# Performance work log

Measured on AMD Instinct MI355X. Metric: run time of the kernel, lower is better.

Reference implementation:

```python
import jax, jax.numpy as jnp
import numpy as np
from jax import lax

B, L, F = 32, 2048, 76   # batch, seq_len, feat_dim
H = 128                  # conv hidden channels
D = 128                  # prototype dim (last 1x1 conv)
P = 128                  # number of prototypes
CLASS_SIZE = 2


def setup_inputs() -> dict:
    key = jax.random.key(0)
    ks = jax.random.split(key, 8)
    w = lambda k, shape: jax.random.normal(k, shape, jnp.float32) * 0.05
    return {
        "x": jax.random.normal(ks[0], (B, L, F), jnp.float32),
        "W1": w(ks[1], (H, F, 5)), "b1": jnp.zeros((H,), jnp.float32),
        "W2": w(ks[2], (H, H, 5)), "b2": jnp.zeros((H,), jnp.float32),
        "W3": w(ks[3], (H, H, 5)), "b3": jnp.zeros((H,), jnp.float32),
        "Wo1": w(ks[4], (D, H)), "bo1": jnp.zeros((D,), jnp.float32),
        "Wo2": w(ks[5], (D, D)), "bo2": jnp.zeros((D,), jnp.float32),
        "prototypes": jax.random.uniform(ks[6], (P, D), jnp.float32),
        "protop_classes": jnp.concatenate([jnp.zeros(P // 2, jnp.int32), jnp.ones(P // 2, jnp.int32)]),
    }


def _conv1d_same(h, W, b):
    # h: (B, C, L), W: (O, C, K=5), symmetric padding 2 == torch padding=k//2
    y = lax.conv_general_dilated(h, W, window_strides=(1,), padding=[(2, 2)],
                                 dimension_numbers=("NCW", "OIW", "NCW"))
    return y + b[None, :, None]


def _maxpool2(h):
    return lax.reduce_window(h, -jnp.inf, lax.max, (1, 1, 2), (1, 1, 2), "VALID")


def reference(x, W1, b1, W2, b2, W3, b3, Wo1, bo1, Wo2, bo2, prototypes, protop_classes):
    h = jnp.transpose(x, (0, 2, 1))  # (B, F, L)
    for W, b in ((W1, b1), (W2, b2), (W3, b3)):
        h = _maxpool2(jax.nn.relu(_conv1d_same(h, W, b)))
    # 1x1 convs as channel matmuls
    h = jax.nn.relu(jnp.einsum("bcl,oc->bol", h, Wo1) + bo1[None, :, None])
    h = jax.nn.relu(jnp.einsum("bcl,oc->bol", h, Wo2) + bo2[None, :, None])
    f = jnp.transpose(h, (0, 2, 1))  # (B, Lp=256, D)
    # l2_conv via ||a-b||^2 = ||a||^2 - 2 a.b + ||b||^2 (same math, GEMM form)
    d2 = (jnp.sum(f * f, axis=-1, keepdims=True)
          - 2.0 * jnp.einsum("bld,pd->blp", f, prototypes)
          + jnp.sum(prototypes * prototypes, axis=-1))  # (B, Lp, P)
    dis = jnp.sqrt(jnp.maximum(d2, 1e-12))
    min_dis = jnp.min(dis, axis=1)  # (B, P): min over patches
    # dis2sim, 'log' activation
    sim = jnp.log((min_dis + 1.0) / (min_dis + 1e-4))
    # init_weights: last_layer.weight[i,j] = 1 if protop_classes[j]==i else -0.5
    lw = jnp.where(protop_classes[None, :] == jnp.arange(CLASS_SIZE)[:, None], 1.0, -0.5)
    out = jax.nn.sigmoid(sim @ lw.T)  # (B, CLASS_SIZE)
    return out, min_dis
```

## Files before the change

### kernel.cpp

```cpp
#include <hip/hip_runtime.h>
#include <cmath>


typedef __attribute__((ext_vector_type(8))) short short8;
typedef __attribute__((ext_vector_type(4))) float f32x4;

__device__ __forceinline__ unsigned short f2bf(float v) {
    union { float f; unsigned u; } x; x.f = v;
    unsigned r = x.u + 0x7fffu + ((x.u >> 16) & 1u);
    return (unsigned short)(r >> 16);
}
__device__ __forceinline__ float bf2f(unsigned short b) {
    union { unsigned u; float f; } x; x.u = ((unsigned)b) << 16;
    return x.f;
}

__device__ void pack_conv_w(int t, int total, const float* __restrict__ W, int C,
                            unsigned short* __restrict__ dst)
{
    if (t >= total) return;
    int lane = t & 63, rest = t >> 6;
    int mf = rest & 7; rest >>= 3;
    int kk = rest % 5, cc = rest / 5;
    int m = mf * 16 + (lane & 15);
    int cb = cc * 32 + (lane >> 4) * 8;
    unsigned short v[8];
#pragma unroll
    for (int j = 0; j < 8; ++j) {
        int c = cb + j;
        v[j] = (c < C) ? f2bf(W[((size_t)m * C + c) * 5 + kk]) : (unsigned short)0;
    }
    *(uint4*)&dst[(size_t)t * 8] = *(uint4*)v;
}

__device__ void pack_mat(int t, const float* __restrict__ M, unsigned short* __restrict__ dst)
{
    if (t >= 2048) return;
    int lane = t & 63, mf = (t >> 6) & 7, cc = t >> 9;
    int m = mf * 16 + (lane & 15);
    int c0 = cc * 32 + (lane >> 4) * 8;
    unsigned short v[8];
#pragma unroll
    for (int j = 0; j < 8; ++j) v[j] = f2bf(M[(size_t)m * 128 + c0 + j]);
    *(uint4*)&dst[(size_t)t * 8] = *(uint4*)v;
}

__global__ __launch_bounds__(256)
void prep_weights_kernel(const float* __restrict__ W1, const float* __restrict__ W2,
                         const float* __restrict__ W3, const float* __restrict__ Wo1,
                         const float* __restrict__ Wo2, const float* __restrict__ protos,
                         unsigned short* A1, unsigned short* A2, unsigned short* A3,
                         unsigned short* AW1, unsigned short* AW2, unsigned short* AP,
                         float* pn, unsigned* pm_bits)
{
    int t = blockIdx.x * 256 + threadIdx.x;
    switch (blockIdx.y) {
    case 0: pack_conv_w(t, 7680,  W1, 76,  A1); break;
    case 1: pack_conv_w(t, 10240, W2, 128, A2); break;
    case 2: pack_conv_w(t, 10240, W3, 128, A3); break;
    case 3: pack_mat(t, Wo1, AW1); break;
    case 4: pack_mat(t, Wo2, AW2); break;
    case 5: pack_mat(t, protos, AP); break;
    case 6:
        if (t < 128) {
            float s = 0.f;
            for (int d = 0; d < 128; ++d) {
                float v = bf2f(f2bf(protos[(size_t)t * 128 + d]));
                s = fmaf(v, v, s);
            }
            pn[t] = s;
        }
        break;
    case 7:
        if (t < 4096) pm_bits[t] = 0x7F800000u;
        break;
    }
}

template <int NM, int NJ, int NCC, int STRIDE, int ROWMAX>
__device__ __forceinline__ void conv_k(const unsigned short* __restrict__ Af,
                                       const unsigned short* __restrict__ sIn,
                                       int nbase, int mf0, int lane,
                                       f32x4 (&acc)[NM][NJ])
{
    const int lc = lane & 15;
    const int lk = (lane >> 4) * 8;
#pragma unroll
    for (int i = 0; i < NM; ++i)
#pragma unroll
        for (int j = 0; j < NJ; ++j) acc[i][j] = (f32x4){0.f, 0.f, 0.f, 0.f};

#pragma unroll
    for (int cc = 0; cc < NCC; ++cc) {
#pragma unroll
        for (int kk = 0; kk < 5; ++kk) {
            const int step = cc * 5 + kk;
            short8 a[NM];
#pragma unroll
            for (int i = 0; i < NM; ++i)
                a[i] = *(const short8*)&Af[(((size_t)step * 8 + mf0 + i) * 64 + lane) * 8];
            short8 bb[NJ];
#pragma unroll
            for (int j = 0; j < NJ; ++j) {
                int row = nbase + j * 16 + lc + kk;
                if (ROWMAX >= 0) row = min(row, ROWMAX);
                bb[j] = *(const short8*)&sIn[row * STRIDE + cc * 32 + lk];
            }
#pragma unroll
            for (int j = 0; j < NJ; ++j)
#pragma unroll
                for (int i = 0; i < NM; ++i)
                    acc[i][j] = __builtin_amdgcn_mfma_f32_16x16x32_bf16(a[i], bb[j], acc[i][j], 0, 0, 0);
        }
    }
}

__device__ __forceinline__ void gemm_head(const unsigned short* __restrict__ Af,
                                          const unsigned short* __restrict__ s_f,
                                          int mf0h, int lane, f32x4 (&acc)[2])
{
    const int lc = lane & 15;
    const int lk = (lane >> 4) * 8;
    acc[0] = (f32x4){0.f, 0.f, 0.f, 0.f};
    acc[1] = (f32x4){0.f, 0.f, 0.f, 0.f};
#pragma unroll
    for (int cc = 0; cc < 4; ++cc) {
        short8 a[2];
#pragma unroll
        for (int i = 0; i < 2; ++i)
            a[i] = *(const short8*)&Af[(((size_t)cc * 8 + mf0h + i) * 64 + lane) * 8];
        short8 bb = *(const short8*)&s_f[lc * 136 + cc * 32 + lk];
#pragma unroll
        for (int i = 0; i < 2; ++i)
            acc[i] = __builtin_amdgcn_mfma_f32_16x16x32_bf16(a[i], bb, acc[i], 0, 0, 0);
    }
}

__global__ __launch_bounds__(256, 4)
void mega_kernel(const float* __restrict__ x,
                 const unsigned short* __restrict__ A1, const float* __restrict__ b1,
                 const unsigned short* __restrict__ A2, const float* __restrict__ b2,
                 const unsigned short* __restrict__ A3, const float* __restrict__ b3,
                 const unsigned short* __restrict__ AW1, const float* __restrict__ bo1,
                 const unsigned short* __restrict__ AW2, const float* __restrict__ bo2,
                 const unsigned short* __restrict__ AP,  const float* __restrict__ pn,
                 unsigned* __restrict__ pm_bits)
{
    __shared__ __align__(16) unsigned short s_x[92 * 84 + 16];
    __shared__ __align__(16) unsigned short s_h1[44 * 136];
    __shared__ float s_cb[768];
    __shared__ float s_part[64];
    __shared__ float s_fn[16];
    unsigned short* s_h2 = s_x;
    unsigned short* s_f  = s_x + 2720;

    const int tid  = threadIdx.x;
    const int u    = blockIdx.x;
    const int b    = blockIdx.y;
    const int lane = tid & 63;
    const int wid  = tid >> 6;
    const int lc   = lane & 15;
    const int lq   = (lane >> 4) * 4;

    for (int i = tid; i < 768; i += 256) {
        const float* src = (i < 128) ? b1 : (i < 256) ? b2 : (i < 384) ? b3
                         : (i < 512) ? bo1 : (i < 640) ? bo2 : pn;
        s_cb[i] = src[i & 127];
    }
    if (tid < 16) s_x[92 * 84 + tid] = 0;

    const int xbase = 64 * u - 14;
    for (int idx = tid; idx < 92 * 21; idx += 256) {
        int pos = idx / 21, c0 = (idx % 21) * 4;
        int l = xbase + pos;
        unsigned short v[4] = {0, 0, 0, 0};
        if (c0 < 76 && l >= 0 && l < 2048) {
            float4 xv = *(const float4*)&x[((size_t)b * 2048 + l) * 76 + c0];
            v[0] = f2bf(xv.x); v[1] = f2bf(xv.y); v[2] = f2bf(xv.z); v[3] = f2bf(xv.w);
        }
        *(uint2*)&s_x[pos * 84 + c0] = *(uint2*)v;
    }
    __syncthreads();

    {
        const int mg = wid & 1, ng = wid >> 1;
        const int mf0 = mg * 4;
        f32x4 acc[4][3];
        conv_k<4, 3, 3, 84, 91>(A1, s_x, ng * 48, mf0, lane, acc);

#pragma unroll
        for (int i = 0; i < 4; ++i) {
            const int ch0 = (mf0 + i) * 16 + lq;
#pragma unroll
            for (int j = 0; j < 3; ++j) {
                const int nl = ng * 48 + j * 16 + lc;
                unsigned short pk[4];
#pragma unroll
                for (int r = 0; r < 4; ++r) {
                    float v = fmaxf(acc[i][j][r] + s_cb[ch0 + r], 0.f);
                    float o = __shfl_xor(v, 1);
                    pk[r] = f2bf(fmaxf(v, o));
                }
                if ((lc & 1) == 0) {
                    int rr = nl >> 1;
                    int jg = 32 * u - 6 + rr;
                    if (rr < 44) {
                        uint2 val = (jg >= 0 && jg < 1024) ? *(uint2*)pk : make_uint2(0u, 0u);
                        *(uint2*)&s_h1[rr * 136 + ch0] = val;
                    }
                }
            }
        }
    }
    __syncthreads();

    {
        const int mf0 = wid * 2;
        f32x4 acc[2][3];
        conv_k<2, 3, 4, 136, 43>(A2, s_h1, 0, mf0, lane, acc);

#pragma unroll
        for (int i = 0; i < 2; ++i) {
            const int ch0 = (mf0 + i) * 16 + lq;
#pragma unroll
            for (int j = 0; j < 3; ++j) {
                const int nl = j * 16 + lc;
                unsigned short pk[4];
#pragma unroll
                for (int r = 0; r < 4; ++r) {
                    float v = fmaxf(acc[i][j][r] + s_cb[128 + ch0 + r], 0.f);
                    float o = __shfl_xor(v, 1);
                    pk[r] = f2bf(fmaxf(v, o));
                }
                if ((lc & 1) == 0) {
                    int rr = nl >> 1;
                    int jg = 16 * u - 2 + rr;
                    if (rr < 20) {
                        uint2 val = (jg >= 0 && jg < 512) ? *(uint2*)pk : make_uint2(0u, 0u);
                        *(uint2*)&s_h2[rr * 136 + ch0] = val;
                    }
                }
            }
        }
    }
    __syncthreads();

    {
        const int mf0 = wid * 2;
        f32x4 acc[2][1];
        conv_k<2, 1, 4, 136, -1>(A3, s_h2, 0, mf0, lane, acc);

#pragma unroll
        for (int i = 0; i < 2; ++i) {
            const int ch0 = (mf0 + i) * 16 + lq;
            unsigned short pk[4];
#pragma unroll
            for (int r = 0; r < 4; ++r) {
                float v = fmaxf(acc[i][0][r] + s_cb[256 + ch0 + r], 0.f);
                float o = __shfl_xor(v, 1);
                pk[r] = f2bf(fmaxf(v, o));
            }
            if ((lc & 1) == 0)
                *(uint2*)&s_f[(lc >> 1) * 136 + ch0] = *(uint2*)pk;
        }
        for (int i = tid; i < 544; i += 256)
            ((unsigned*)(s_f + 1088))[i] = 0u;
    }
    __syncthreads();

    const int mf0h = wid * 2;
    f32x4 hacc[2];

    gemm_head(AW1, s_f, mf0h, lane, hacc);
    __syncthreads();
#pragma unroll
    for (int i = 0; i < 2; ++i) {
        const int ch0 = (mf0h + i) * 16 + lq;
        unsigned short pk[4];
#pragma unroll
        for (int r = 0; r < 4; ++r)
            pk[r] = f2bf(fmaxf(hacc[i][r] + s_cb[384 + ch0 + r], 0.f));
        *(uint2*)&s_f[lc * 136 + ch0] = *(uint2*)pk;
    }
    __syncthreads();

    gemm_head(AW2, s_f, mf0h, lane, hacc);
    __syncthreads();
#pragma unroll
    for (int i = 0; i < 2; ++i) {
        const int ch0 = (mf0h + i) * 16 + lq;
        unsigned short pk[4];
#pragma unroll
        for (int r = 0; r < 4; ++r)
            pk[r] = f2bf(fmaxf(hacc[i][r] + s_cb[512 + ch0 + r], 0.f));
        *(uint2*)&s_f[lc * 136 + ch0] = *(uint2*)pk;
    }
    __syncthreads();

    if (tid < 64) {
        int n = tid >> 2, part = tid & 3;
        float s = 0.f;
        for (int c = part * 32; c < part * 32 + 32; ++c) {
            float v = bf2f(s_f[n * 136 + c]);
            s = fmaf(v, v, s);
        }
        s_part[part * 16 + n] = s;
    }
    __syncthreads();
    if (tid < 16)
        s_fn[tid] = s_part[tid] + s_part[16 + tid] + s_part[32 + tid] + s_part[48 + tid];
    __syncthreads();

    gemm_head(AP, s_f, mf0h, lane, hacc);

#pragma unroll
    for (int i = 0; i < 2; ++i) {
#pragma unroll
        for (int r = 0; r < 4; ++r) {
            const int p = (mf0h + i) * 16 + lq + r;
            float d2 = s_fn[lc] + s_cb[640 + p] - 2.f * hacc[i][r];
            float m = (lc < 8) ? sqrtf(fmaxf(d2, 1e-12f)) : 3.0e38f;
#pragma unroll
            for (int s = 1; s < 16; s <<= 1)
                m = fminf(m, __shfl_xor(m, s));
            if (lc == 0)
                atomicMin(&pm_bits[(size_t)b * 128 + p], __float_as_uint(m));
        }
    }
}

__global__ __launch_bounds__(128)
void finalize_kernel(const float* __restrict__ pm,
                     const int* __restrict__ classes,
                     float* __restrict__ out)
{
    __shared__ float r0[128], r1[128];
    const int b = blockIdx.x, p = threadIdx.x;
    float m = pm[(size_t)b * 128 + p];
    out[64 + b * 128 + p] = m;

    float sim = logf((m + 1.0f) / (m + 1e-4f));
    int cls = classes[p];
    r0[p] = (cls == 0) ? sim : -0.5f * sim;
    r1[p] = (cls == 1) ? sim : -0.5f * sim;
    __syncthreads();
    for (int s = 64; s > 0; s >>= 1) {
        if (p < s) { r0[p] += r0[p + s]; r1[p] += r1[p + s]; }
        __syncthreads();
    }
    if (p == 0) {
        out[b * 2 + 0] = 1.f / (1.f + expf(-r0[0]));
        out[b * 2 + 1] = 1.f / (1.f + expf(-r1[0]));
    }
}

extern "C" void kernel_launch(void* const* d_in, const int* in_sizes, int n_in,
                              void* d_out, int out_size, void* d_ws, size_t ws_size,
                              hipStream_t stream)
{
    (void)in_sizes; (void)n_in; (void)out_size; (void)ws_size;
    const float* x    = (const float*)d_in[0];
    const float* W1   = (const float*)d_in[1];
    const float* b1   = (const float*)d_in[2];
    const float* W2   = (const float*)d_in[3];
    const float* b2   = (const float*)d_in[4];
    const float* W3   = (const float*)d_in[5];
    const float* b3   = (const float*)d_in[6];
    const float* Wo1  = (const float*)d_in[7];
    const float* bo1  = (const float*)d_in[8];
    const float* Wo2  = (const float*)d_in[9];
    const float* bo2  = (const float*)d_in[10];
    const float* prot = (const float*)d_in[11];
    const int*   cls  = (const int*)d_in[12];
    float* out = (float*)d_out;

    char* ws = (char*)d_ws;
    unsigned short* A1  = (unsigned short*)(ws);
    unsigned short* A2  = (unsigned short*)(ws + 122880);
    unsigned short* A3  = (unsigned short*)(ws + 286720);
    unsigned short* AW1 = (unsigned short*)(ws + 450560);
    unsigned short* AW2 = (unsigned short*)(ws + 483328);
    unsigned short* AP  = (unsigned short*)(ws + 516096);
    float*          pn  = (float*)(ws + 548864);
    unsigned*       pm  = (unsigned*)(ws + 549376);

    prep_weights_kernel<<<dim3(40, 8), 256, 0, stream>>>(W1, W2, W3, Wo1, Wo2, prot,
                                                         A1, A2, A3, AW1, AW2, AP, pn, pm);
    mega_kernel<<<dim3(32, 32), 256, 0, stream>>>(x, A1, b1, A2, b2, A3, b3,
                                                  AW1, bo1, AW2, bo2, AP, pn, pm);
    finalize_kernel<<<32, 128, 0, stream>>>((const float*)pm, cls, out);
}
```

Measured before the change: 139.7 us.

## Split fused mega-kernel into per-layer conv kernels with global bf16 intermediates

Replaces the single fused kernel, which recomputed halo regions in shared memory, with separate kernels. One converts x to padded bf16, then one kernel each runs conv1, conv2, and conv3 plus the head, with intermediates kept in global memory and zeroed padding rows. This removes redundant halo computation and enlarges per-warp MFMA tiles. The cost is extra launches, global round-trips of activations, operand loads from global memory instead of LDS, and smaller grids that may underfill the GPU.

Measured after the change: 155.2 us. +11.1%, slower.

```diff
diff --git a/kernel.cpp b/kernel.cpp
--- a/kernel.cpp
+++ b/kernel.cpp
@@ -13,6 +13,21 @@
 __device__ __forceinline__ float bf2f(unsigned short b) {
     union { unsigned u; float f; } x; x.u = ((unsigned)b) << 16;
     return x.f;
+}
+
+__global__ __launch_bounds__(256)
+void convert_x_kernel(const float* __restrict__ x, unsigned short* __restrict__ xb)
+{
+    int t = blockIdx.x * 256 + threadIdx.x;
+    int row = t / 12, c0 = (t % 12) * 8;
+    int b = row >> 11, p = row & 2047;
+    unsigned short v[8];
+#pragma unroll
+    for (int j = 0; j < 8; ++j) {
+        int c = c0 + j;
+        v[j] = (c < 76) ? f2bf(x[((size_t)b * 2048 + p) * 76 + c]) : (unsigned short)0;
+    }
+    *(uint4*)&xb[((size_t)b * 2052 + p + 2) * 96 + c0] = *(uint4*)v;
 }
 
 __device__ void pack_conv_w(int t, int total, const float* __restrict__ W, int C,
@@ -51,7 +66,8 @@
                          const float* __restrict__ Wo2, const float* __restrict__ protos,
                          unsigned short* A1, unsigned short* A2, unsigned short* A3,
                          unsigned short* AW1, unsigned short* AW2, unsigned short* AP,
-                         float* pn, unsigned* pm_bits)
+                         float* pn, unsigned* pm_bits,
+                         unsigned* xb_u, unsigned* h1_u, unsigned* h2_u)
 {
     int t = blockIdx.x * 256 + threadIdx.x;
     switch (blockIdx.y) {
@@ -74,17 +90,32 @@
     case 7:
         if (t < 4096) pm_bits[t] = 0x7F800000u;
         break;
-    }
-}
-
-template <int NM, int NJ, int NCC, int STRIDE, int ROWMAX>
-__device__ __forceinline__ void conv_k(const unsigned short* __restrict__ Af,
-                                       const unsigned short* __restrict__ sIn,
-                                       int nbase, int mf0, int lane,
-                                       f32x4 (&acc)[NM][NJ])
-{
-    const int lc = lane & 15;
-    const int lk = (lane >> 4) * 8;
+    case 8: {
+        for (int i = t; i < 32 * 4 * 48; i += 10240) {
+            int b = i / 192, rem = i % 192, rr = rem / 48, c2 = rem % 48;
+            int r = (rr < 2) ? rr : 2048 + rr;
+            xb_u[((size_t)b * 2052 + r) * 48 + c2] = 0u;
+        }
+        for (int i = t; i < 32 * 4 * 64; i += 10240) {
+            int b = i / 256, rem = i % 256, rr = rem / 64, c2 = rem % 64;
+            int r = (rr < 2) ? rr : 1024 + rr;
+            h1_u[((size_t)b * 1028 + r) * 64 + c2] = 0u;
+        }
+        for (int i = t; i < 32 * 4 * 64; i += 10240) {
+            int b = i / 256, rem = i % 256, rr = rem / 64, c2 = rem % 64;
+            int r = (rr < 2) ? rr : 512 + rr;
+            h2_u[((size_t)b * 516 + r) * 64 + c2] = 0u;
+        }
+        break;
+    }
+    }
+}
+
+template <int NM, int NJ, int NCC, int RSTRIDE>
+__device__ __forceinline__ void conv_g(const unsigned short* __restrict__ Af,
+                                       const unsigned short* __restrict__ Bbase,
+                                       int mf0, int lane, f32x4 (&acc)[NM][NJ])
+{
 #pragma unroll
     for (int i = 0; i < NM; ++i)
 #pragma unroll
@@ -101,11 +132,8 @@
                 a[i] = *(const short8*)&Af[(((size_t)step * 8 + mf0 + i) * 64 + lane) * 8];
             short8 bb[NJ];
 #pragma unroll
-            for (int j = 0; j < NJ; ++j) {
-                int row = nbase + j * 16 + lc + kk;
-                if (ROWMAX >= 0) row = min(row, ROWMAX);
-                bb[j] = *(const short8*)&sIn[row * STRIDE + cc * 32 + lk];
-            }
+            for (int j = 0; j < NJ; ++j)
+                bb[j] = *(const short8*)&Bbase[(size_t)(j * 16 + kk) * RSTRIDE + cc * 32];
 #pragma unroll
             for (int j = 0; j < NJ; ++j)
 #pragma unroll
@@ -115,172 +143,162 @@
     }
 }
 
-__device__ __forceinline__ void gemm_head(const unsigned short* __restrict__ Af,
-                                          const unsigned short* __restrict__ s_f,
-                                          int mf0h, int lane, f32x4 (&acc)[2])
+template <int NM, int NJ>
+__device__ __forceinline__ void conv_epilogue(f32x4 (&acc)[NM][NJ],
+                                              const float* __restrict__ bias,
+                                              unsigned short* __restrict__ out,
+                                              size_t outbase,
+                                              int p0, int mf0, int lane)
 {
     const int lc = lane & 15;
-    const int lk = (lane >> 4) * 8;
-    acc[0] = (f32x4){0.f, 0.f, 0.f, 0.f};
-    acc[1] = (f32x4){0.f, 0.f, 0.f, 0.f};
-#pragma unroll
-    for (int cc = 0; cc < 4; ++cc) {
-        short8 a[2];
-#pragma unroll
-        for (int i = 0; i < 2; ++i)
-            a[i] = *(const short8*)&Af[(((size_t)cc * 8 + mf0h + i) * 64 + lane) * 8];
-        short8 bb = *(const short8*)&s_f[lc * 136 + cc * 32 + lk];
-#pragma unroll
-        for (int i = 0; i < 2; ++i)
-            acc[i] = __builtin_amdgcn_mfma_f32_16x16x32_bf16(a[i], bb, acc[i], 0, 0, 0);
-    }
-}
-
-__global__ __launch_bounds__(256, 4)
-void mega_kernel(const float* __restrict__ x,
-                 const unsigned short* __restrict__ A1, const float* __restrict__ b1,
-                 const unsigned short* __restrict__ A2, const float* __restrict__ b2,
-                 const unsigned short* __restrict__ A3, const float* __restrict__ b3,
-                 const unsigned short* __restrict__ AW1, const float* __restrict__ bo1,
-                 const unsigned short* __restrict__ AW2, const float* __restrict__ bo2,
-                 const unsigned short* __restrict__ AP,  const float* __restrict__ pn,
-                 unsigned* __restrict__ pm_bits)
-{
-    __shared__ __align__(16) unsigned short s_x[92 * 84 + 16];
-    __shared__ __align__(16) unsigned short s_h1[44 * 136];
-    __shared__ float s_cb[768];
-    __shared__ float s_part[64];
-    __shared__ float s_fn[16];
-    unsigned short* s_h2 = s_x;
-    unsigned short* s_f  = s_x + 2720;
-
-    const int tid  = threadIdx.x;
-    const int u    = blockIdx.x;
-    const int b    = blockIdx.y;
-    const int lane = tid & 63;
-    const int wid  = tid >> 6;
-    const int lc   = lane & 15;
-    const int lq   = (lane >> 4) * 4;
-
-    for (int i = tid; i < 768; i += 256) {
-        const float* src = (i < 128) ? b1 : (i < 256) ? b2 : (i < 384) ? b3
-                         : (i < 512) ? bo1 : (i < 640) ? bo2 : pn;
-        s_cb[i] = src[i & 127];
-    }
-    if (tid < 16) s_x[92 * 84 + tid] = 0;
-
-    const int xbase = 64 * u - 14;
-    for (int idx = tid; idx < 92 * 21; idx += 256) {
-        int pos = idx / 21, c0 = (idx % 21) * 4;
-        int l = xbase + pos;
-        unsigned short v[4] = {0, 0, 0, 0};
-        if (c0 < 76 && l >= 0 && l < 2048) {
-            float4 xv = *(const float4*)&x[((size_t)b * 2048 + l) * 76 + c0];
-            v[0] = f2bf(xv.x); v[1] = f2bf(xv.y); v[2] = f2bf(xv.z); v[3] = f2bf(xv.w);
-        }
-        *(uint2*)&s_x[pos * 84 + c0] = *(uint2*)v;
-    }
-    __syncthreads();
-
-    {
-        const int mg = wid & 1, ng = wid >> 1;
-        const int mf0 = mg * 4;
-        f32x4 acc[4][3];
-        conv_k<4, 3, 3, 84, 91>(A1, s_x, ng * 48, mf0, lane, acc);
-
-#pragma unroll
-        for (int i = 0; i < 4; ++i) {
-            const int ch0 = (mf0 + i) * 16 + lq;
-#pragma unroll
-            for (int j = 0; j < 3; ++j) {
-                const int nl = ng * 48 + j * 16 + lc;
-                unsigned short pk[4];
-#pragma unroll
-                for (int r = 0; r < 4; ++r) {
-                    float v = fmaxf(acc[i][j][r] + s_cb[ch0 + r], 0.f);
-                    float o = __shfl_xor(v, 1);
-                    pk[r] = f2bf(fmaxf(v, o));
-                }
-                if ((lc & 1) == 0) {
-                    int rr = nl >> 1;
-                    int jg = 32 * u - 6 + rr;
-                    if (rr < 44) {
-                        uint2 val = (jg >= 0 && jg < 1024) ? *(uint2*)pk : make_uint2(0u, 0u);
-                        *(uint2*)&s_h1[rr * 136 + ch0] = val;
-                    }
-                }
-            }
-        }
-    }
-    __syncthreads();
-
-    {
-        const int mf0 = wid * 2;
-        f32x4 acc[2][3];
-        conv_k<2, 3, 4, 136, 43>(A2, s_h1, 0, mf0, lane, acc);
-
-#pragma unroll
-        for (int i = 0; i < 2; ++i) {
-            const int ch0 = (mf0 + i) * 16 + lq;
-#pragma unroll
-            for (int j = 0; j < 3; ++j) {
-                const int nl = j * 16 + lc;
-                unsigned short pk[4];
-#pragma unroll
-                for (int r = 0; r < 4; ++r) {
-                    float v = fmaxf(acc[i][j][r] + s_cb[128 + ch0 + r], 0.f);
-                    float o = __shfl_xor(v, 1);
-                    pk[r] = f2bf(fmaxf(v, o));
-                }
-                if ((lc & 1) == 0) {
-                    int rr = nl >> 1;
-                    int jg = 16 * u - 2 + rr;
-                    if (rr < 20) {
-                        uint2 val = (jg >= 0 && jg < 512) ? *(uint2*)pk : make_uint2(0u, 0u);
-                        *(uint2*)&s_h2[rr * 136 + ch0] = val;
-                    }
-                }
-            }
-        }
-    }
-    __syncthreads();
-
-    {
-        const int mf0 = wid * 2;
-        f32x4 acc[2][1];
-        conv_k<2, 1, 4, 136, -1>(A3, s_h2, 0, mf0, lane, acc);
-
-#pragma unroll
-        for (int i = 0; i < 2; ++i) {
-            const int ch0 = (mf0 + i) * 16 + lq;
+    const int lq = (lane >> 4) * 4;
+#pragma unroll
+    for (int i = 0; i < NM; ++i) {
+        const int ch0 = (mf0 + i) * 16 + lq;
+        const float4 bi = *(const float4*)&bias[ch0];
+        const float bv[4] = {bi.x, bi.y, bi.z, bi.w};
+#pragma unroll
+        for (int j = 0; j < NJ; ++j) {
+            const int p = p0 + j * 16 + lc;
             unsigned short pk[4];
 #pragma unroll
             for (int r = 0; r < 4; ++r) {
-                float v = fmaxf(acc[i][0][r] + s_cb[256 + ch0 + r], 0.f);
+                float v = fmaxf(acc[i][j][r] + bv[r], 0.f);
                 float o = __shfl_xor(v, 1);
                 pk[r] = f2bf(fmaxf(v, o));
             }
             if ((lc & 1) == 0)
-                *(uint2*)&s_f[(lc >> 1) * 136 + ch0] = *(uint2*)pk;
-        }
-        for (int i = tid; i < 544; i += 256)
-            ((unsigned*)(s_f + 1088))[i] = 0u;
+                *(uint2*)&out[outbase + (size_t)(p >> 1) * 128 + ch0] = *(uint2*)pk;
+        }
+    }
+}
+
+__global__ __launch_bounds__(256, 2)
+void conv1_kernel(const unsigned short* __restrict__ xb,
+                  const unsigned short* __restrict__ A1,
+                  const float* __restrict__ b1, unsigned short* __restrict__ h1)
+{
+    const int tid = threadIdx.x, lane = tid & 63, wid = tid >> 6;
+    const int mg = wid & 1, ng = wid >> 1, mf0 = mg * 4;
+    const int b = blockIdx.y;
+    const int p0 = blockIdx.x * 128 + ng * 64;
+    const int lc = lane & 15, lk = (lane >> 4) * 8;
+
+    const unsigned short* Bbase = xb + ((size_t)b * 2052 + p0 + lc) * 96 + lk;
+    f32x4 acc[4][4];
+    conv_g<4, 4, 3, 96>(A1, Bbase, mf0, lane, acc);
+    conv_epilogue<4, 4>(acc, b1, h1, ((size_t)b * 1028 + 2) * 128, p0, mf0, lane);
+}
+
+__global__ __launch_bounds__(256, 2)
+void conv2_kernel(const unsigned short* __restrict__ h1,
+                  const unsigned short* __restrict__ A2,
+                  const float* __restrict__ b2, unsigned short* __restrict__ h2)
+{
+    const int tid = threadIdx.x, lane = tid & 63, wid = tid >> 6;
+    const int mg = wid & 1, ng = wid >> 1, mf0 = mg * 4;
+    const int b = blockIdx.y;
+    const int p0 = blockIdx.x * 128 + ng * 64;
+    const int lc = lane & 15, lk = (lane >> 4) * 8;
+
+    const unsigned short* Bbase = h1 + ((size_t)b * 1028 + p0 + lc) * 128 + lk;
+    f32x4 acc[4][4];
+    conv_g<4, 4, 4, 128>(A2, Bbase, mf0, lane, acc);
+    conv_epilogue<4, 4>(acc, b2, h2, ((size_t)b * 516 + 2) * 128, p0, mf0, lane);
+}
+
+__device__ __forceinline__ void gemm_head(const unsigned short* __restrict__ Af,
+                                          const unsigned short* __restrict__ s_f,
+                                          int mf0h, int lane, f32x4 (&acc)[2][2])
+{
+    const int lc = lane & 15;
+    const int lk = (lane >> 4) * 8;
+#pragma unroll
+    for (int i = 0; i < 2; ++i)
+#pragma unroll
+        for (int j = 0; j < 2; ++j) acc[i][j] = (f32x4){0.f, 0.f, 0.f, 0.f};
+#pragma unroll
+    for (int cc = 0; cc < 4; ++cc) {
+        short8 a[2];
+#pragma unroll
+        for (int i = 0; i < 2; ++i)
+            a[i] = *(const short8*)&Af[(((size_t)cc * 8 + mf0h + i) * 64 + lane) * 8];
+        short8 bb[2];
+#pragma unroll
+        for (int j = 0; j < 2; ++j)
+            bb[j] = *(const short8*)&s_f[(j * 16 + lc) * 136 + cc * 32 + lk];
+#pragma unroll
+        for (int i = 0; i < 2; ++i)
+#pragma unroll
+            for (int j = 0; j < 2; ++j)
+                acc[i][j] = __builtin_amdgcn_mfma_f32_16x16x32_bf16(a[i], bb[j], acc[i][j], 0, 0, 0);
+    }
+}
+
+__global__ __launch_bounds__(256, 2)
+void conv3_head_kernel(const unsigned short* __restrict__ h2,
+                       const unsigned short* __restrict__ A3, const float* __restrict__ b3,
+                       const unsigned short* __restrict__ AW1, const float* __restrict__ bo1,
+                       const unsigned short* __restrict__ AW2, const float* __restrict__ bo2,
+                       const unsigned short* __restrict__ AP,  const float* __restrict__ pn,
+                       unsigned* __restrict__ pm_bits)
+{
+    __shared__ __align__(16) unsigned short s_f[32 * 136];
+    __shared__ float s_part[4 * 32];
+    __shared__ float s_fn[32];
+
+    const int tid = threadIdx.x, lane = tid & 63, wid = tid >> 6;
+    const int b = blockIdx.y;
+    const int lc = lane & 15, lk = (lane >> 4) * 8;
+    const int lq = (lane >> 4) * 4;
+
+    {
+        const int mg = wid & 1, ng = wid >> 1, mf0 = mg * 4;
+        const int p0 = blockIdx.x * 64 + ng * 32;
+        const unsigned short* Bbase = h2 + ((size_t)b * 516 + p0 + lc) * 128 + lk;
+        f32x4 acc[4][2];
+        conv_g<4, 2, 4, 128>(A3, Bbase, mf0, lane, acc);
+
+#pragma unroll
+        for (int i = 0; i < 4; ++i) {
+            const int ch0 = (mf0 + i) * 16 + lq;
+            const float4 bi = *(const float4*)&b3[ch0];
+            const float bv[4] = {bi.x, bi.y, bi.z, bi.w};
+#pragma unroll
+            for (int j = 0; j < 2; ++j) {
+                const int p = p0 + j * 16 + lc;
+                unsigned short pk[4];
+#pragma unroll
+                for (int r = 0; r < 4; ++r) {
+                    float v = fmaxf(acc[i][j][r] + bv[r], 0.f);
+                    float o = __shfl_xor(v, 1);
+                    pk[r] = f2bf(fmaxf(v, o));
+                }
+                if ((lc & 1) == 0)
+                    *(uint2*)&s_f[(size_t)((p >> 1) - blockIdx.x * 32) * 136 + ch0] = *(uint2*)pk;
+            }
+        }
     }
     __syncthreads();
 
     const int mf0h = wid * 2;
-    f32x4 hacc[2];
+    f32x4 hacc[2][2];
 
     gemm_head(AW1, s_f, mf0h, lane, hacc);
     __syncthreads();
 #pragma unroll
     for (int i = 0; i < 2; ++i) {
         const int ch0 = (mf0h + i) * 16 + lq;
-        unsigned short pk[4];
-#pragma unroll
-        for (int r = 0; r < 4; ++r)
-            pk[r] = f2bf(fmaxf(hacc[i][r] + s_cb[384 + ch0 + r], 0.f));
-        *(uint2*)&s_f[lc * 136 + ch0] = *(uint2*)pk;
+        const float4 bi = *(const float4*)&bo1[ch0];
+        const float bv[4] = {bi.x, bi.y, bi.z, bi.w};
+#pragma unroll
+        for (int j = 0; j < 2; ++j) {
+            unsigned short pk[4];
+#pragma unroll
+            for (int r = 0; r < 4; ++r)
+                pk[r] = f2bf(fmaxf(hacc[i][j][r] + bv[r], 0.f));
+            *(uint2*)&s_f[(j * 16 + lc) * 136 + ch0] = *(uint2*)pk;
+        }
     }
     __syncthreads();
 
@@ -289,26 +307,31 @@
 #pragma unroll
     for (int i = 0; i < 2; ++i) {
         const int ch0 = (mf0h + i) * 16 + lq;
-        unsigned short pk[4];
-#pragma unroll
-        for (int r = 0; r < 4; ++r)
-            pk[r] = f2bf(fmaxf(hacc[i][r] + s_cb[512 + ch0 + r], 0.f));
-        *(uint2*)&s_f[lc * 136 + ch0] = *(uint2*)pk;
-    }
-    __syncthreads();
-
-    if (tid < 64) {
-        int n = tid >> 2, part = tid & 3;
+        const float4 bi = *(const float4*)&bo2[ch0];
+        const float bv[4] = {bi.x, bi.y, bi.z, bi.w};
+#pragma unroll
+        for (int j = 0; j < 2; ++j) {
+            unsigned short pk[4];
+#pragma unroll
+            for (int r = 0; r < 4; ++r)
+                pk[r] = f2bf(fmaxf(hacc[i][j][r] + bv[r], 0.f));
+            *(uint2*)&s_f[(j * 16 + lc) * 136 + ch0] = *(uint2*)pk;
+        }
+    }
+    __syncthreads();
+
+    if (tid < 128) {
+        int n = tid & 31, part = tid >> 5;
         float s = 0.f;
         for (int c = part * 32; c < part * 32 + 32; ++c) {
             float v = bf2f(s_f[n * 136 + c]);
             s = fmaf(v, v, s);
         }
-        s_part[part * 16 + n] = s;
-    }
-    __syncthreads();
-    if (tid < 16)
-        s_fn[tid] = s_part[tid] + s_part[16 + tid] + s_part[32 + tid] + s_part[48 + tid];
+        s_part[part * 32 + n] = s;
+    }
+    __syncthreads();
+    if (tid < 32)
+        s_fn[tid] = s_part[tid] + s_part[32 + tid] + s_part[64 + tid] + s_part[96 + tid];
     __syncthreads();
 
     gemm_head(AP, s_f, mf0h, lane, hacc);
@@ -318,8 +341,14 @@
 #pragma unroll
         for (int r = 0; r < 4; ++r) {
             const int p = (mf0h + i) * 16 + lq + r;
-            float d2 = s_fn[lc] + s_cb[640 + p] - 2.f * hacc[i][r];
-            float m = (lc < 8) ? sqrtf(fmaxf(d2, 1e-12f)) : 3.0e38f;
+            const float pnp = pn[p];
+            float m = 3.0e38f;
+#pragma unroll
+            for (int j = 0; j < 2; ++j) {
+                const int n = j * 16 + lc;
+                float d2 = s_fn[n] + pnp - 2.f * hacc[i][j][r];
+                m = fminf(m, sqrtf(fmaxf(d2, 1e-12f)));
+            }
 #pragma unroll
             for (int s = 1; s < 16; s <<= 1)
                 m = fminf(m, __shfl_xor(m, s));
@@ -375,18 +404,26 @@
     float* out = (float*)d_out;
 
     char* ws = (char*)d_ws;
-    unsigned short* A1  = (unsigned short*)(ws);
-    unsigned short* A2  = (unsigned short*)(ws + 122880);
-    unsigned short* A3  = (unsigned short*)(ws + 286720);
-    unsigned short* AW1 = (unsigned short*)(ws + 450560);
-    unsigned short* AW2 = (unsigned short*)(ws + 483328);
-    unsigned short* AP  = (unsigned short*)(ws + 516096);
-    float*          pn  = (float*)(ws + 548864);
-    unsigned*       pm  = (unsigned*)(ws + 549376);
-
-    prep_weights_kernel<<<dim3(40, 8), 256, 0, stream>>>(W1, W2, W3, Wo1, Wo2, prot,
-                                                         A1, A2, A3, AW1, AW2, AP, pn, pm);
-    mega_kernel<<<dim3(32, 32), 256, 0, stream>>>(x, A1, b1, A2, b2, A3, b3,
-                                                  AW1, bo1, AW2, bo2, AP, pn, pm);
+    unsigned short* xb = (unsigned short*)(ws);
+    unsigned short* h1 = (unsigned short*)(ws + 12607488);
+    unsigned short* h2 = (unsigned short*)(ws + 21028864);
+    const size_t FR = 25296896;
+    unsigned short* A1  = (unsigned short*)(ws + FR);
+    unsigned short* A2  = (unsigned short*)(ws + FR + 122880);
+    unsigned short* A3  = (unsigned short*)(ws + FR + 286720);
+    unsigned short* AW1 = (unsigned short*)(ws + FR + 450560);
+    unsigned short* AW2 = (unsigned short*)(ws + FR + 483328);
+    unsigned short* AP  = (unsigned short*)(ws + FR + 516096);
+    float*          pn  = (float*)(ws + FR + 548864);
+    unsigned*       pm  = (unsigned*)(ws + FR + 549376);
+
+    convert_x_kernel<<<3072, 256, 0, stream>>>(x, xb);
+    prep_weights_kernel<<<dim3(40, 9), 256, 0, stream>>>(W1, W2, W3, Wo1, Wo2, prot,
+                                                         A1, A2, A3, AW1, AW2, AP, pn, pm,
+                                                         (unsigned*)xb, (unsigned*)h1, (unsigned*)h2);
+    conv1_kernel<<<dim3(16, 32), 256, 0, stream>>>(xb, A1, b1, h1);
+    conv2_kernel<<<dim3(8, 32), 256, 0, stream>>>(h1, A2, b2, h2);
+    conv3_head_kernel<<<dim3(8, 32), 256, 0, stream>>>(h2, A3, b3, AW1, bo1, AW2, bo2,
+                                                       AP, pn, pm);
     finalize_kernel<<<32, 128, 0, stream>>>((const float*)pm, cls, out);
 }
```
